# Kernel tuning notes

Measured on AMD Instinct MI355X. Metric: run time of the kernel, lower is better.

## Reference

```python
import jax, jax.numpy as jnp
import numpy as np

NEG_SLOPE = 0.2  # negative_slope of LeakyReLU

def _leaky_relu(x):
    return jnp.where(x >= 0, x, NEG_SLOPE * x)

def setup_inputs() -> dict:
    key = jax.random.key(0)
    ks = jax.random.split(key, 8)
    n_s, n_t, n_edges = 100000, 25000, 1600000
    d_s_in = d_t_in = 256
    d_s_out = d_t_out = 256
    x_source = jax.random.normal(ks[0], (n_s, d_s_in), jnp.float32)
    x_target = jax.random.normal(ks[1], (n_t, d_t_in), jnp.float32)
    # sparse neighborhood N: [n_target, n_source], COO (row=target i, col=source j)
    edge_row = jax.random.randint(ks[2], (n_edges,), 0, n_t)
    edge_col = jax.random.randint(ks[3], (n_edges,), 0, n_s)
    n_vals = jax.random.uniform(ks[4], (n_edges,), jnp.float32)
    # learnable parameters (xavier-uniform-ish scale)
    w_s = jax.random.normal(ks[5], (d_s_in, d_t_out), jnp.float32) * 0.074  # [source_in, target_out]
    w_t = jax.random.normal(ks[6], (d_t_in, d_s_out), jnp.float32) * 0.074  # [target_in, source_out]
    att_weight = jax.random.normal(ks[7], (d_t_out + d_s_out,), jnp.float32) * 0.074
    return {"x_source": x_source, "x_target": x_target, "n_vals": n_vals,
            "w_s": w_s, "w_t": w_t, "att_weight": att_weight,
            "edge_row": edge_row, "edge_col": edge_col}

def reference(x_source, x_target, n_vals, w_s, w_t, att_weight, edge_row, edge_col):
    n_s = x_source.shape[0]
    n_t = x_target.shape[0]
    d_t_out = w_s.shape[1]  # target_out_channels (split point of att_weight)
    s_msg = x_source @ w_s  # [n_s, target_out]
    t_msg = x_target @ w_t  # [n_t, source_out]
    # e_ij = LeakyReLU([s_msg_j || t_msg_i] @ a); factor the linear part per node
    a1 = att_weight[:d_t_out]   # acts on s_msg part
    a2 = att_weight[d_t_out:]   # acts on t_msg part
    p_s = s_msg @ a1            # [n_s]
    p_t = t_msg @ a2            # [n_t]
    # f on the transposed edge (i'=source=col, j'=target=row) with permuted weight
    # [a2 || a1] gives p_t[row] + p_s[col]: identical per-edge scores as e.
    ev = _leaky_relu(p_s[edge_col] + p_t[edge_row])  # [E]
    # sparse_row_norm (softmax=False): divide by row sums
    rowsum_t = jax.ops.segment_sum(ev, edge_row, num_segments=n_t)  # rows of N
    rowsum_s = jax.ops.segment_sum(ev, edge_col, num_segments=n_s)  # rows of N^T
    att_s = ev / rowsum_t[edge_row]  # A_s, aligned with N
    att_t = ev / rowsum_s[edge_col]  # A_t, aligned with N^T
    # Hadamard with N values, then sparse-dense matmul (scatter-add)
    w_e = n_vals * att_s
    w_f = n_vals * att_t
    message_on_target = jax.ops.segment_sum(w_e[:, None] * s_msg[edge_col], edge_row, num_segments=n_t)  # Y_t
    message_on_source = jax.ops.segment_sum(w_f[:, None] * t_msg[edge_row], edge_col, num_segments=n_s)  # Y_s
    # update_func=None -> identity
    return message_on_source, message_on_target
```

## Files before the change

kernel.cpp:

```cpp
#include <hip/hip_runtime.h>

#define D 256

typedef float f32x4 __attribute__((ext_vector_type(4)));

#define PROWS 32
#define PSTRIDE (D + 4)

__global__ __launch_bounds__(256) void fused_p_all(
        const float* __restrict__ xs, const float* __restrict__ ws,
        float* __restrict__ ps, unsigned short* __restrict__ xbs, int n_s, int nblk_s,
        const float* __restrict__ xt, const float* __restrict__ wt,
        float* __restrict__ pt, unsigned short* __restrict__ xbt, int n_t,
        const float* __restrict__ att) {
    __shared__ float sbuf[PROWS][PSTRIDE];
    const float* X; const float* W; float* p; unsigned short* xb;
    int M, att_off, row0;
    if (blockIdx.x < nblk_s) {
        X = xs; W = ws; p = ps; xb = xbs; M = n_s; att_off = 0;
        row0 = blockIdx.x * PROWS;
    } else {
        X = xt; W = wt; p = pt; xb = xbt; M = n_t; att_off = D;
        row0 = (blockIdx.x - nblk_s) * PROWS;
    }
    const int tid = threadIdx.x;
    for (int idx = tid; idx < PROWS * (D / 4); idx += 256) {
        int r = idx >> 6;
        int c4 = (idx & 63) * 4;
        int grow = row0 + r;
        int srcrow = grow < M ? grow : M - 1;
        *reinterpret_cast<float4*>(&sbuf[r][c4]) =
            *reinterpret_cast<const float4*>(X + (size_t)srcrow * D + c4);
    }
    __syncthreads();

    if (xb) {
        const int half = tid >> 7;
        const int c2 = (tid & 127) * 2;
        for (int r = half; r < PROWS; r += 2) {
            int row = row0 + r;
            if (row < M) {
                unsigned int u0 = __float_as_uint(sbuf[r][c2]);
                unsigned int u1 = __float_as_uint(sbuf[r][c2 + 1]);
                u0 = (u0 + 0x7FFFu + ((u0 >> 16) & 1u)) >> 16;
                u1 = (u1 + 0x7FFFu + ((u1 >> 16) & 1u)) >> 16;
                unsigned int packed = (u1 << 16) | (u0 & 0xFFFFu);
                *reinterpret_cast<unsigned int*>(xb + (size_t)row * D + c2) = packed;
            }
        }
    }

    const int g = tid >> 6;
    const int l = tid & 63;
    const int r0 = g * 8;
    float acc[8][4];
    #pragma unroll
    for (int r = 0; r < 8; ++r)
        #pragma unroll
        for (int q = 0; q < 4; ++q) acc[r][q] = 0.f;

    const float* wbase = W + 4 * l;
    for (int k8 = 0; k8 < D; k8 += 8) {
        float4 wv[8];
        #pragma unroll
        for (int kk = 0; kk < 8; ++kk)
            wv[kk] = *reinterpret_cast<const float4*>(wbase + (size_t)(k8 + kk) * D);
        #pragma unroll
        for (int h = 0; h < 2; ++h) {
            float4 xv[8];
            #pragma unroll
            for (int r = 0; r < 8; ++r)
                xv[r] = *reinterpret_cast<const float4*>(&sbuf[r0 + r][k8 + 4 * h]);
            #pragma unroll
            for (int kk = 0; kk < 4; ++kk) {
                float4 w4 = wv[4 * h + kk];
                #pragma unroll
                for (int r = 0; r < 8; ++r) {
                    float xsc = (kk == 0) ? xv[r].x : (kk == 1) ? xv[r].y
                              : (kk == 2) ? xv[r].z : xv[r].w;
                    acc[r][0] = __fmaf_rn(xsc, w4.x, acc[r][0]);
                    acc[r][1] = __fmaf_rn(xsc, w4.y, acc[r][1]);
                    acc[r][2] = __fmaf_rn(xsc, w4.z, acc[r][2]);
                    acc[r][3] = __fmaf_rn(xsc, w4.w, acc[r][3]);
                }
            }
        }
    }
    __syncthreads();
    #pragma unroll
    for (int r = 0; r < 8; ++r)
        *reinterpret_cast<float4*>(&sbuf[r0 + r][4 * l]) =
            make_float4(acc[r][0], acc[r][1], acc[r][2], acc[r][3]);
    __syncthreads();
    if (tid < PROWS) {
        int row = row0 + tid;
        if (row < M) {
            float s = 0.f;
            const float* ap = att + att_off;
            for (int j = 0; j < D; ++j) s = __fmaf_rn(sbuf[tid][j], ap[j], s);
            p[row] = s;
        }
    }
}

__global__ void count_kernel(const int* __restrict__ er, const int* __restrict__ ec,
                             int* __restrict__ cnt_t, int* __restrict__ cnt_s, int ne) {
    int e = blockIdx.x * blockDim.x + threadIdx.x;
    int st = gridDim.x * blockDim.x;
    for (; e < ne; e += st) {
        atomicAdd(&cnt_t[er[e]], 1);
        atomicAdd(&cnt_s[ec[e]], 1);
    }
}

__device__ void scan_body(const int* __restrict__ cnt, int* __restrict__ off, int n) {
    const int VPT = 16;
    __shared__ int wsum[4];
    __shared__ int s_carry;
    const int tid = threadIdx.x;
    const int lane = tid & 63, wv = tid >> 6;
    if (tid == 0) s_carry = 0;
    __syncthreads();
    for (int base = 0; base < n; base += 256 * VPT) {
        int v[VPT];
        int idx0 = base + tid * VPT;
        int tsum = 0;
        #pragma unroll
        for (int k = 0; k < VPT; ++k) {
            int id = idx0 + k;
            v[k] = (id < n) ? cnt[id] : 0;
            tsum += v[k];
        }
        int x = tsum;
        #pragma unroll
        for (int o = 1; o < 64; o <<= 1) {
            int y = __shfl_up(x, o, 64);
            if (lane >= o) x += y;
        }
        if (lane == 63) wsum[wv] = x;
        __syncthreads();
        int woff = 0;
        for (int w = 0; w < 4; ++w) if (w < wv) woff += wsum[w];
        int excl = s_carry + woff + x - tsum;
        int run = excl;
        #pragma unroll
        for (int k = 0; k < VPT; ++k) {
            int id = idx0 + k;
            if (id < n) off[id] = run;
            run += v[k];
        }
        __syncthreads();
        if (tid == 255) s_carry = excl + tsum;
        __syncthreads();
    }
    if (tid == 0) off[n] = s_carry;
}

__global__ __launch_bounds__(256) void scan2_kernel(const int* __restrict__ cnt_t,
        int* __restrict__ off_t, int n_t, const int* __restrict__ cnt_s,
        int* __restrict__ off_s, int n_s) {
    if (blockIdx.x == 0) scan_body(cnt_t, off_t, n_t);
    else scan_body(cnt_s, off_s, n_s);
}

__global__ void fill_kernel(const int* __restrict__ er, const int* __restrict__ ec,
                            const int* __restrict__ off_t, const int* __restrict__ off_s,
                            int* __restrict__ cur_t, int* __restrict__ cur_s,
                            int* __restrict__ list_t, int* __restrict__ list_s, int ne) {
    int e = blockIdx.x * blockDim.x + threadIdx.x;
    int st = gridDim.x * blockDim.x;
    for (; e < ne; e += st) {
        int r = er[e];
        int p1 = atomicAdd(&cur_t[r], 1);
        list_t[off_t[r] + p1] = e;
        int c = ec[e];
        int p2 = atomicAdd(&cur_s[c], 1);
        list_s[off_s[c] + p2] = e;
    }
}

#define MAXD 160

__global__ __launch_bounds__(64) void rowsum_weight_all(
        const int* __restrict__ off_t, int* __restrict__ list_t,
        const int* __restrict__ ecol,
        const float* __restrict__ p_t, const float* __restrict__ p_s,
        float* __restrict__ wlist_t, int n_t,
        const int* __restrict__ off_s, int* __restrict__ list_s,
        const int* __restrict__ erow,
        float* __restrict__ wlist_s, int n_s,
        const float* __restrict__ nv) {
    __shared__ int raw[MAXD];
    __shared__ int so[MAXD];
    __shared__ float sev[MAXD];
    __shared__ float snv[MAXD];
    const int bid = blockIdx.x;
    const int* off; int* list; const int* other_idx;
    const float* p_own; const float* p_other; float* wlist; int row;
    if (bid < n_t) { off = off_t; list = list_t; other_idx = ecol;
                     p_own = p_t; p_other = p_s; wlist = wlist_t; row = bid; }
    else           { off = off_s; list = list_s; other_idx = erow;
                     p_own = p_s; p_other = p_t; wlist = wlist_s; row = bid - n_t; }
    const int lane = threadIdx.x;
    const int b = off[row];
    int deg = off[row + 1] - b;
    if (deg > MAXD) deg = MAXD;

    for (int i = lane; i < deg; i += 64) raw[i] = list[b + i];
    __syncthreads();
    int myv[(MAXD + 63) / 64], myr[(MAXD + 63) / 64];
    #pragma unroll
    for (int c = 0; c < (MAXD + 63) / 64; ++c) {
        int i = lane + c * 64;
        if (i < deg) {
            int v = raw[i];
            int rank = 0;
            for (int j = 0; j < deg; ++j) rank += (raw[j] < v);
            myv[c] = v; myr[c] = rank;
        }
    }
    __syncthreads();
    #pragma unroll
    for (int c = 0; c < (MAXD + 63) / 64; ++c) {
        int i = lane + c * 64;
        if (i < deg) raw[myr[c]] = myv[c];
    }
    __syncthreads();
    const float po = p_own[row];
    for (int i = lane; i < deg; i += 64) {
        int e = raw[i];
        int o = other_idx[e];
        so[i] = o;
        float t = __fadd_rn(p_other[o], po);
        sev[i] = (t >= 0.f) ? t : __fmul_rn(0.2f, t);
        snv[i] = nv[e];
    }
    __syncthreads();
    float rs = 0.f;
    for (int i = 0; i < deg; ++i) rs = __fadd_rn(rs, sev[i]);
    for (int i = lane; i < deg; i += 64) {
        list[b + i]  = so[i];
        wlist[b + i] = __fmul_rn(snv[i], __fdiv_rn(sev[i], rs));
    }
}

__global__ __launch_bounds__(256) void gather_all_bf16(
        const int* __restrict__ off_t, const int* __restrict__ olist_t,
        const float* __restrict__ wlist_t, const unsigned short* __restrict__ xb_s,
        float* __restrict__ out_tgt, int n_t,
        const int* __restrict__ off_s, const int* __restrict__ olist_s,
        const float* __restrict__ wlist_s, const unsigned short* __restrict__ xb_t,
        float* __restrict__ out_src, int n_s) {
    const int gid = blockIdx.x * 4 + (threadIdx.x >> 6);
    if (gid >= n_t + n_s) return;
    const int lane = threadIdx.x & 63;
    const int* off; const int* ol; const float* wl;
    const unsigned short* xo; float* out; int row;
    if (gid < n_t) { off = off_t; ol = olist_t; wl = wlist_t;
                     xo = xb_s; out = out_tgt; row = gid; }
    else           { off = off_s; ol = olist_s; wl = wlist_s;
                     xo = xb_t; out = out_src; row = gid - n_t; }
    const int b = off[row];
    const int end = off[row + 1];
    const size_t eoff = (size_t)lane * 4;

    float ax = 0.f, ay = 0.f, az = 0.f, aw = 0.f;
    int i = b;
    for (; i + 8 <= end; i += 8) {
        int o[8]; float w[8]; uint2 xv[8];
        #pragma unroll
        for (int u = 0; u < 8; ++u) { o[u] = ol[i + u]; w[u] = wl[i + u]; }
        #pragma unroll
        for (int u = 0; u < 8; ++u)
            xv[u] = *reinterpret_cast<const uint2*>(xo + (size_t)o[u] * D + eoff);
        #pragma unroll
        for (int u = 0; u < 8; ++u) {
            float x0 = __uint_as_float(xv[u].x << 16);
            float x1 = __uint_as_float(xv[u].x & 0xFFFF0000u);
            float x2 = __uint_as_float(xv[u].y << 16);
            float x3 = __uint_as_float(xv[u].y & 0xFFFF0000u);
            ax = fmaf(w[u], x0, ax); ay = fmaf(w[u], x1, ay);
            az = fmaf(w[u], x2, az); aw = fmaf(w[u], x3, aw);
        }
    }
    for (; i < end; ++i) {
        int o = ol[i];
        float w = wl[i];
        uint2 xv = *reinterpret_cast<const uint2*>(xo + (size_t)o * D + eoff);
        float x0 = __uint_as_float(xv.x << 16);
        float x1 = __uint_as_float(xv.x & 0xFFFF0000u);
        float x2 = __uint_as_float(xv.y << 16);
        float x3 = __uint_as_float(xv.y & 0xFFFF0000u);
        ax = fmaf(w, x0, ax); ay = fmaf(w, x1, ay);
        az = fmaf(w, x2, az); aw = fmaf(w, x3, aw);
    }
    f32x4 r = {ax, ay, az, aw};
    __builtin_nontemporal_store(r,
        reinterpret_cast<f32x4*>(out + (size_t)row * D + eoff));
}

#define BAND 32
#define KT 8

__global__ __launch_bounds__(256) void band_gemm_all(
        float* __restrict__ Cs, const float* __restrict__ Bs_w, int nblk_s, int Ms,
        float* __restrict__ Ct, const float* __restrict__ Bt_w, int Mt) {
    __shared__ float Xs[BAND][D];
    __shared__ float Bs[KT][D];
    float* C; const float* B; int M, base_row;
    if (blockIdx.x < nblk_s) { C = Cs; B = Bs_w; M = Ms; base_row = blockIdx.x * BAND; }
    else { C = Ct; B = Bt_w; M = Mt; base_row = (blockIdx.x - nblk_s) * BAND; }
    const int tid = threadIdx.x;
    const int r0 = (tid >> 5) * 4;
    const int cA = (tid & 31) * 4;

    for (int s = tid; s < BAND * (D / 4); s += 256) {
        int row = s >> 6;
        int c4 = (s & 63) * 4;
        int grow = base_row + row;
        int srow = grow < M ? grow : M - 1;
        f32x4 v = __builtin_nontemporal_load(
            reinterpret_cast<const f32x4*>(C + (size_t)srow * D + c4));
        *reinterpret_cast<f32x4*>(&Xs[row][c4]) = v;
    }

    float acc[4][8];
    #pragma unroll
    for (int i = 0; i < 4; ++i)
        #pragma unroll
        for (int j = 0; j < 8; ++j) acc[i][j] = 0.f;

    for (int kt = 0; kt < D; kt += KT) {
        __syncthreads();
        for (int s = tid; s < KT * (D / 4); s += 256) {
            int row = s >> 6;
            int c4 = (s & 63) * 4;
            *reinterpret_cast<float4*>(&Bs[row][c4]) =
                *reinterpret_cast<const float4*>(B + (size_t)(kt + row) * D + c4);
        }
        __syncthreads();
        #pragma unroll
        for (int k4 = 0; k4 < KT; k4 += 4) {
            float4 av[4];
            #pragma unroll
            for (int i = 0; i < 4; ++i)
                av[i] = *reinterpret_cast<const float4*>(&Xs[r0 + i][kt + k4]);
            #pragma unroll
            for (int kk = 0; kk < 4; ++kk) {
                float4 blo = *reinterpret_cast<const float4*>(&Bs[k4 + kk][cA]);
                float4 bhi = *reinterpret_cast<const float4*>(&Bs[k4 + kk][cA + 128]);
                #pragma unroll
                for (int i = 0; i < 4; ++i) {
                    float a = (kk == 0) ? av[i].x : (kk == 1) ? av[i].y
                            : (kk == 2) ? av[i].z : av[i].w;
                    acc[i][0] = fmaf(a, blo.x, acc[i][0]);
                    acc[i][1] = fmaf(a, blo.y, acc[i][1]);
                    acc[i][2] = fmaf(a, blo.z, acc[i][2]);
                    acc[i][3] = fmaf(a, blo.w, acc[i][3]);
                    acc[i][4] = fmaf(a, bhi.x, acc[i][4]);
                    acc[i][5] = fmaf(a, bhi.y, acc[i][5]);
                    acc[i][6] = fmaf(a, bhi.z, acc[i][6]);
                    acc[i][7] = fmaf(a, bhi.w, acc[i][7]);
                }
            }
        }
    }
    #pragma unroll
    for (int i = 0; i < 4; ++i) {
        int row = base_row + r0 + i;
        if (row < M) {
            float* cp = C + (size_t)row * D;
            f32x4 lo = {acc[i][0], acc[i][1], acc[i][2], acc[i][3]};
            f32x4 hi = {acc[i][4], acc[i][5], acc[i][6], acc[i][7]};
            __builtin_nontemporal_store(lo, reinterpret_cast<f32x4*>(cp + cA));
            __builtin_nontemporal_store(hi, reinterpret_cast<f32x4*>(cp + cA + 128));
        }
    }
}

extern "C" void kernel_launch(void* const* d_in, const int* in_sizes, int n_in,
                              void* d_out, int out_size, void* d_ws, size_t ws_size,
                              hipStream_t stream) {
    const float* x_s = (const float*)d_in[0];
    const float* x_t = (const float*)d_in[1];
    const float* nv  = (const float*)d_in[2];
    const float* w_s = (const float*)d_in[3];
    const float* w_t = (const float*)d_in[4];
    const float* att = (const float*)d_in[5];
    const int* erow  = (const int*)d_in[6];
    const int* ecol  = (const int*)d_in[7];

    const int n_s = in_sizes[0] / D;
    const int n_t = in_sizes[1] / D;
    const int ne  = in_sizes[6];

    float* p_s      = (float*)d_ws;
    float* p_t      = p_s + n_s;
    float* wlist_t  = p_t + n_t;
    float* wlist_s  = wlist_t + ne;
    int* cnt_t  = (int*)(wlist_s + ne);
    int* cnt_s  = cnt_t + n_t;
    int* off_t  = cnt_s + n_s;
    int* off_s  = off_t + (n_t + 1);
    int* list_t = off_s + (n_s + 1);
    int* list_s = list_t + ne;
    unsigned short* xb_s = (unsigned short*)(list_s + ne);
    unsigned short* xb_t = xb_s + (size_t)n_s * D;
    size_t need = (size_t)((char*)(xb_t + (size_t)n_t * D) - (char*)d_ws);
    const bool use_bf16 = ws_size >= need;

    float* out_src = (float*)d_out;
    float* out_tgt = out_src + (size_t)n_s * D;

    (void)hipMemsetAsync(cnt_t, 0, (size_t)(n_t + n_s) * sizeof(int), stream);

    const int pblk_s = (n_s + PROWS - 1) / PROWS;
    const int pblk_t = (n_t + PROWS - 1) / PROWS;
    fused_p_all<<<pblk_s + pblk_t, 256, 0, stream>>>(
        x_s, w_s, p_s, use_bf16 ? xb_s : nullptr, n_s, pblk_s,
        x_t, w_t, p_t, use_bf16 ? xb_t : nullptr, n_t, att);

    count_kernel<<<2048, 256, 0, stream>>>(erow, ecol, cnt_t, cnt_s, ne);
    scan2_kernel<<<2, 256, 0, stream>>>(cnt_t, off_t, n_t, cnt_s, off_s, n_s);
    (void)hipMemsetAsync(cnt_t, 0, (size_t)(n_t + n_s) * sizeof(int), stream);
    fill_kernel<<<2048, 256, 0, stream>>>(erow, ecol, off_t, off_s, cnt_t, cnt_s,
                                          list_t, list_s, ne);

    rowsum_weight_all<<<n_t + n_s, 64, 0, stream>>>(off_t, list_t, ecol, p_t, p_s,
                                                    wlist_t, n_t,
                                                    off_s, list_s, erow,
                                                    wlist_s, n_s, nv);

    if (use_bf16) {
        int rows = n_t + n_s;
        gather_all_bf16<<<(rows + 3) / 4, 256, 0, stream>>>(
            off_t, list_t, wlist_t, xb_s, out_tgt, n_t,
            off_s, list_s, wlist_s, xb_t, out_src, n_s);
    }

    const int gblk_s = (n_s + BAND - 1) / BAND;
    const int gblk_t = (n_t + BAND - 1) / BAND;
    band_gemm_all<<<gblk_s + gblk_t, 256, 0, stream>>>(out_src, w_t, gblk_s, n_s,
                                                       out_tgt, w_s, n_t);
}
```

Baseline: 1.186 ms.

## Fuse edge counting into projection kernel and drop second memset

Merges the edge degree-count atomics into the projection/p-score kernel: extra leading blocks do the counting, so it overlaps with the dense projection work and one launch disappears. The projection tile shrinks to 16 rows per block with a launch-bounds occupancy hint, and fill now uses separate cursor arrays zeroed by a single larger memset, which removes the second memset between kernels. Streaming reads of edge lists and weights switch to nontemporal loads. The smaller tile reloads W more often per row, and the count blocks compete with projection blocks for CUs.

Result: slower. 1.300 ms (+9.6%).

```diff
diff --git a/kernel.cpp b/kernel.cpp
--- a/kernel.cpp
+++ b/kernel.cpp
@@ -4,24 +4,36 @@
 
 typedef float f32x4 __attribute__((ext_vector_type(4)));
 
-#define PROWS 32
+#define PROWS 16
 #define PSTRIDE (D + 4)
 
-__global__ __launch_bounds__(256) void fused_p_all(
+__global__ __launch_bounds__(256, 6) void fused_p_count(
         const float* __restrict__ xs, const float* __restrict__ ws,
         float* __restrict__ ps, unsigned short* __restrict__ xbs, int n_s, int nblk_s,
         const float* __restrict__ xt, const float* __restrict__ wt,
         float* __restrict__ pt, unsigned short* __restrict__ xbt, int n_t,
-        const float* __restrict__ att) {
+        const float* __restrict__ att,
+        const int* __restrict__ er, const int* __restrict__ ec,
+        int* __restrict__ cnt_t, int* __restrict__ cnt_s, int ne, int cb) {
     __shared__ float sbuf[PROWS][PSTRIDE];
+    if (blockIdx.x < (unsigned)cb) {
+        int e = blockIdx.x * 256 + threadIdx.x;
+        int st = cb * 256;
+        for (; e < ne; e += st) {
+            atomicAdd(&cnt_t[er[e]], 1);
+            atomicAdd(&cnt_s[ec[e]], 1);
+        }
+        return;
+    }
+    const int pbid = blockIdx.x - cb;
     const float* X; const float* W; float* p; unsigned short* xb;
     int M, att_off, row0;
-    if (blockIdx.x < nblk_s) {
+    if (pbid < nblk_s) {
         X = xs; W = ws; p = ps; xb = xbs; M = n_s; att_off = 0;
-        row0 = blockIdx.x * PROWS;
+        row0 = pbid * PROWS;
     } else {
         X = xt; W = wt; p = pt; xb = xbt; M = n_t; att_off = D;
-        row0 = (blockIdx.x - nblk_s) * PROWS;
+        row0 = (pbid - nblk_s) * PROWS;
     }
     const int tid = threadIdx.x;
     for (int idx = tid; idx < PROWS * (D / 4); idx += 256) {
@@ -52,10 +64,10 @@
 
     const int g = tid >> 6;
     const int l = tid & 63;
-    const int r0 = g * 8;
-    float acc[8][4];
-    #pragma unroll
-    for (int r = 0; r < 8; ++r)
+    const int r0 = g * 4;
+    float acc[4][4];
+    #pragma unroll
+    for (int r = 0; r < 4; ++r)
         #pragma unroll
         for (int q = 0; q < 4; ++q) acc[r][q] = 0.f;
 
@@ -67,15 +79,15 @@
             wv[kk] = *reinterpret_cast<const float4*>(wbase + (size_t)(k8 + kk) * D);
         #pragma unroll
         for (int h = 0; h < 2; ++h) {
-            float4 xv[8];
+            float4 xv[4];
             #pragma unroll
-            for (int r = 0; r < 8; ++r)
+            for (int r = 0; r < 4; ++r)
                 xv[r] = *reinterpret_cast<const float4*>(&sbuf[r0 + r][k8 + 4 * h]);
             #pragma unroll
             for (int kk = 0; kk < 4; ++kk) {
                 float4 w4 = wv[4 * h + kk];
                 #pragma unroll
-                for (int r = 0; r < 8; ++r) {
+                for (int r = 0; r < 4; ++r) {
                     float xsc = (kk == 0) ? xv[r].x : (kk == 1) ? xv[r].y
                               : (kk == 2) ? xv[r].z : xv[r].w;
                     acc[r][0] = __fmaf_rn(xsc, w4.x, acc[r][0]);
@@ -88,7 +100,7 @@
     }
     __syncthreads();
     #pragma unroll
-    for (int r = 0; r < 8; ++r)
+    for (int r = 0; r < 4; ++r)
         *reinterpret_cast<float4*>(&sbuf[r0 + r][4 * l]) =
             make_float4(acc[r][0], acc[r][1], acc[r][2], acc[r][3]);
     __syncthreads();
@@ -100,16 +112,6 @@
             for (int j = 0; j < D; ++j) s = __fmaf_rn(sbuf[tid][j], ap[j], s);
             p[row] = s;
         }
-    }
-}
-
-__global__ void count_kernel(const int* __restrict__ er, const int* __restrict__ ec,
-                             int* __restrict__ cnt_t, int* __restrict__ cnt_s, int ne) {
-    int e = blockIdx.x * blockDim.x + threadIdx.x;
-    int st = gridDim.x * blockDim.x;
-    for (; e < ne; e += st) {
-        atomicAdd(&cnt_t[er[e]], 1);
-        atomicAdd(&cnt_s[ec[e]], 1);
     }
 }
 
@@ -206,7 +208,8 @@
     int deg = off[row + 1] - b;
     if (deg > MAXD) deg = MAXD;
 
-    for (int i = lane; i < deg; i += 64) raw[i] = list[b + i];
+    for (int i = lane; i < deg; i += 64)
+        raw[i] = __builtin_nontemporal_load(list + b + i);
     __syncthreads();
     int myv[(MAXD + 63) / 64], myr[(MAXD + 63) / 64];
     #pragma unroll
@@ -233,7 +236,7 @@
         so[i] = o;
         float t = __fadd_rn(p_other[o], po);
         sev[i] = (t >= 0.f) ? t : __fmul_rn(0.2f, t);
-        snv[i] = nv[e];
+        snv[i] = __builtin_nontemporal_load(nv + e);
     }
     __syncthreads();
     float rs = 0.f;
@@ -269,7 +272,10 @@
     for (; i + 8 <= end; i += 8) {
         int o[8]; float w[8]; uint2 xv[8];
         #pragma unroll
-        for (int u = 0; u < 8; ++u) { o[u] = ol[i + u]; w[u] = wl[i + u]; }
+        for (int u = 0; u < 8; ++u) {
+            o[u] = __builtin_nontemporal_load(ol + i + u);
+            w[u] = __builtin_nontemporal_load(wl + i + u);
+        }
         #pragma unroll
         for (int u = 0; u < 8; ++u)
             xv[u] = *reinterpret_cast<const uint2*>(xo + (size_t)o[u] * D + eoff);
@@ -308,7 +314,7 @@
     __shared__ float Xs[BAND][D];
     __shared__ float Bs[KT][D];
     float* C; const float* B; int M, base_row;
-    if (blockIdx.x < nblk_s) { C = Cs; B = Bs_w; M = Ms; base_row = blockIdx.x * BAND; }
+    if (blockIdx.x < (unsigned)nblk_s) { C = Cs; B = Bs_w; M = Ms; base_row = blockIdx.x * BAND; }
     else { C = Ct; B = Bt_w; M = Mt; base_row = (blockIdx.x - nblk_s) * BAND; }
     const int tid = threadIdx.x;
     const int r0 = (tid >> 5) * 4;
@@ -400,7 +406,9 @@
     float* wlist_s  = wlist_t + ne;
     int* cnt_t  = (int*)(wlist_s + ne);
     int* cnt_s  = cnt_t + n_t;
-    int* off_t  = cnt_s + n_s;
+    int* cur_t  = cnt_s + n_s;
+    int* cur_s  = cur_t + n_t;
+    int* off_t  = cur_s + n_s;
     int* off_s  = off_t + (n_t + 1);
     int* list_t = off_s + (n_s + 1);
     int* list_s = list_t + ne;
@@ -412,18 +420,18 @@
     float* out_src = (float*)d_out;
     float* out_tgt = out_src + (size_t)n_s * D;
 
-    (void)hipMemsetAsync(cnt_t, 0, (size_t)(n_t + n_s) * sizeof(int), stream);
+    (void)hipMemsetAsync(cnt_t, 0, 2 * (size_t)(n_t + n_s) * sizeof(int), stream);
 
     const int pblk_s = (n_s + PROWS - 1) / PROWS;
     const int pblk_t = (n_t + PROWS - 1) / PROWS;
-    fused_p_all<<<pblk_s + pblk_t, 256, 0, stream>>>(
+    const int CB = 1024;
+    fused_p_count<<<CB + pblk_s + pblk_t, 256, 0, stream>>>(
         x_s, w_s, p_s, use_bf16 ? xb_s : nullptr, n_s, pblk_s,
-        x_t, w_t, p_t, use_bf16 ? xb_t : nullptr, n_t, att);
-
-    count_kernel<<<2048, 256, 0, stream>>>(erow, ecol, cnt_t, cnt_s, ne);
+        x_t, w_t, p_t, use_bf16 ? xb_t : nullptr, n_t, att,
+        erow, ecol, cnt_t, cnt_s, ne, CB);
+
     scan2_kernel<<<2, 256, 0, stream>>>(cnt_t, off_t, n_t, cnt_s, off_s, n_s);
-    (void)hipMemsetAsync(cnt_t, 0, (size_t)(n_t + n_s) * sizeof(int), stream);
-    fill_kernel<<<2048, 256, 0, stream>>>(erow, ecol, off_t, off_s, cnt_t, cnt_s,
+    fill_kernel<<<2048, 256, 0, stream>>>(erow, ecol, off_t, off_s, cur_t, cur_s,
                                           list_t, list_s, ne);
 
     rowsum_weight_all<<<n_t + n_s, 64, 0, stream>>>(off_t, list_t, ecol, p_t, p_s,
```

## Parallelize offset scan across tiles and batch gather index loads via wave shuffles

Applied to the files above, without the earlier changes.

Replaces the two-block serial prefix scan with a three-phase tiled scan (tile sums, tiny serial scan of tile sums, per-tile scan) spread over many blocks. Separate cursor arrays are zeroed alongside the counts in one memset, which removes the second memset. The gather kernel now loads 64 neighbor indices and weights per wave cooperatively and broadcasts them with shuffles, unrolling by 16 to keep more row loads in flight. Nontemporal loads are added for streaming list reads. The cost is two extra kernel launches and some shuffle overhead.

Measured after the change: 1.150 ms. 1.03x faster.

```diff
diff --git a/kernel.cpp b/kernel.cpp
--- a/kernel.cpp
+++ b/kernel.cpp
@@ -16,7 +16,7 @@
     __shared__ float sbuf[PROWS][PSTRIDE];
     const float* X; const float* W; float* p; unsigned short* xb;
     int M, att_off, row0;
-    if (blockIdx.x < nblk_s) {
+    if (blockIdx.x < (unsigned)nblk_s) {
         X = xs; W = ws; p = ps; xb = xbs; M = n_s; att_off = 0;
         row0 = blockIdx.x * PROWS;
     } else {
@@ -113,25 +113,72 @@
     }
 }
 
-__device__ void scan_body(const int* __restrict__ cnt, int* __restrict__ off, int n) {
-    const int VPT = 16;
+#define STILE 4096
+
+__global__ __launch_bounds__(256) void scanA_kernel(
+        const int* __restrict__ cnt_t, int n_t,
+        const int* __restrict__ cnt_s, int n_s,
+        int* __restrict__ tsum, int tilesT) {
+    __shared__ int wsum[4];
+    const int tid = threadIdx.x;
+    const int* src; int n, base;
+    if ((int)blockIdx.x < tilesT) { src = cnt_t; n = n_t; base = blockIdx.x * STILE; }
+    else { src = cnt_s; n = n_s; base = (blockIdx.x - tilesT) * STILE; }
+    int s = 0;
+    for (int it = 0; it < STILE; it += 1024) {
+        int idx = base + it + tid * 4;
+        if (idx + 3 < n) {
+            int4 v = *reinterpret_cast<const int4*>(src + idx);
+            s += v.x + v.y + v.z + v.w;
+        } else {
+            #pragma unroll
+            for (int k = 0; k < 4; ++k) if (idx + k < n) s += src[idx + k];
+        }
+    }
+    #pragma unroll
+    for (int o = 32; o > 0; o >>= 1) s += __shfl_xor(s, o, 64);
+    if ((tid & 63) == 0) wsum[tid >> 6] = s;
+    __syncthreads();
+    if (tid == 0) tsum[blockIdx.x] = wsum[0] + wsum[1] + wsum[2] + wsum[3];
+}
+
+__global__ void scanB_kernel(int* __restrict__ tsum, int tilesT, int tilesS,
+                             int* __restrict__ off_t, int n_t,
+                             int* __restrict__ off_s, int n_s, int ne) {
+    if (threadIdx.x == 0) {
+        int run = 0;
+        for (int i = 0; i < tilesT; ++i) { int v = tsum[i]; tsum[i] = run; run += v; }
+        run = 0;
+        for (int i = 0; i < tilesS; ++i) { int v = tsum[tilesT + i]; tsum[tilesT + i] = run; run += v; }
+        off_t[n_t] = ne;
+        off_s[n_s] = ne;
+    }
+}
+
+__global__ __launch_bounds__(256) void scanC_kernel(
+        const int* __restrict__ cnt_t, int n_t, int* __restrict__ off_t,
+        const int* __restrict__ cnt_s, int n_s, int* __restrict__ off_s,
+        const int* __restrict__ tsum, int tilesT) {
     __shared__ int wsum[4];
     __shared__ int s_carry;
     const int tid = threadIdx.x;
     const int lane = tid & 63, wv = tid >> 6;
-    if (tid == 0) s_carry = 0;
-    __syncthreads();
-    for (int base = 0; base < n; base += 256 * VPT) {
-        int v[VPT];
-        int idx0 = base + tid * VPT;
-        int tsum = 0;
-        #pragma unroll
-        for (int k = 0; k < VPT; ++k) {
-            int id = idx0 + k;
-            v[k] = (id < n) ? cnt[id] : 0;
-            tsum += v[k];
-        }
-        int x = tsum;
+    const int* src; int* dst; int n, base;
+    if ((int)blockIdx.x < tilesT) { src = cnt_t; dst = off_t; n = n_t; base = blockIdx.x * STILE; }
+    else { src = cnt_s; dst = off_s; n = n_s; base = (blockIdx.x - tilesT) * STILE; }
+    if (tid == 0) s_carry = tsum[blockIdx.x];
+    __syncthreads();
+    for (int it = 0; it < STILE; it += 1024) {
+        int idx = base + it + tid * 4;
+        int4 v = make_int4(0, 0, 0, 0);
+        if (idx + 3 < n) v = *reinterpret_cast<const int4*>(src + idx);
+        else {
+            if (idx < n)     v.x = src[idx];
+            if (idx + 1 < n) v.y = src[idx + 1];
+            if (idx + 2 < n) v.z = src[idx + 2];
+        }
+        int t4 = v.x + v.y + v.z + v.w;
+        int x = t4;
         #pragma unroll
         for (int o = 1; o < 64; o <<= 1) {
             int y = __shfl_up(x, o, 64);
@@ -141,26 +188,22 @@
         __syncthreads();
         int woff = 0;
         for (int w = 0; w < 4; ++w) if (w < wv) woff += wsum[w];
-        int excl = s_carry + woff + x - tsum;
-        int run = excl;
-        #pragma unroll
-        for (int k = 0; k < VPT; ++k) {
-            int id = idx0 + k;
-            if (id < n) off[id] = run;
-            run += v[k];
+        int excl = s_carry + woff + x - t4;
+        int4 outv;
+        outv.x = excl;
+        outv.y = excl + v.x;
+        outv.z = excl + v.x + v.y;
+        outv.w = excl + v.x + v.y + v.z;
+        if (idx + 3 < n) *reinterpret_cast<int4*>(dst + idx) = outv;
+        else {
+            if (idx < n)     dst[idx] = outv.x;
+            if (idx + 1 < n) dst[idx + 1] = outv.y;
+            if (idx + 2 < n) dst[idx + 2] = outv.z;
         }
         __syncthreads();
-        if (tid == 255) s_carry = excl + tsum;
+        if (tid == 255) s_carry = excl + t4;
         __syncthreads();
     }
-    if (tid == 0) off[n] = s_carry;
-}
-
-__global__ __launch_bounds__(256) void scan2_kernel(const int* __restrict__ cnt_t,
-        int* __restrict__ off_t, int n_t, const int* __restrict__ cnt_s,
-        int* __restrict__ off_s, int n_s) {
-    if (blockIdx.x == 0) scan_body(cnt_t, off_t, n_t);
-    else scan_body(cnt_s, off_s, n_s);
 }
 
 __global__ void fill_kernel(const int* __restrict__ er, const int* __restrict__ ec,
@@ -206,7 +249,8 @@
     int deg = off[row + 1] - b;
     if (deg > MAXD) deg = MAXD;
 
-    for (int i = lane; i < deg; i += 64) raw[i] = list[b + i];
+    for (int i = lane; i < deg; i += 64)
+        raw[i] = __builtin_nontemporal_load(list + b + i);
     __syncthreads();
     int myv[(MAXD + 63) / 64], myr[(MAXD + 63) / 64];
     #pragma unroll
@@ -233,7 +277,7 @@
         so[i] = o;
         float t = __fadd_rn(p_other[o], po);
         sev[i] = (t >= 0.f) ? t : __fmul_rn(0.2f, t);
-        snv[i] = nv[e];
+        snv[i] = __builtin_nontemporal_load(nv + e);
     }
     __syncthreads();
     float rs = 0.f;
@@ -265,34 +309,43 @@
     const size_t eoff = (size_t)lane * 4;
 
     float ax = 0.f, ay = 0.f, az = 0.f, aw = 0.f;
-    int i = b;
-    for (; i + 8 <= end; i += 8) {
-        int o[8]; float w[8]; uint2 xv[8];
-        #pragma unroll
-        for (int u = 0; u < 8; ++u) { o[u] = ol[i + u]; w[u] = wl[i + u]; }
-        #pragma unroll
-        for (int u = 0; u < 8; ++u)
-            xv[u] = *reinterpret_cast<const uint2*>(xo + (size_t)o[u] * D + eoff);
-        #pragma unroll
-        for (int u = 0; u < 8; ++u) {
-            float x0 = __uint_as_float(xv[u].x << 16);
-            float x1 = __uint_as_float(xv[u].x & 0xFFFF0000u);
-            float x2 = __uint_as_float(xv[u].y << 16);
-            float x3 = __uint_as_float(xv[u].y & 0xFFFF0000u);
-            ax = fmaf(w[u], x0, ax); ay = fmaf(w[u], x1, ay);
-            az = fmaf(w[u], x2, az); aw = fmaf(w[u], x3, aw);
-        }
-    }
-    for (; i < end; ++i) {
-        int o = ol[i];
-        float w = wl[i];
-        uint2 xv = *reinterpret_cast<const uint2*>(xo + (size_t)o * D + eoff);
-        float x0 = __uint_as_float(xv.x << 16);
-        float x1 = __uint_as_float(xv.x & 0xFFFF0000u);
-        float x2 = __uint_as_float(xv.y << 16);
-        float x3 = __uint_as_float(xv.y & 0xFFFF0000u);
-        ax = fmaf(w, x0, ax); ay = fmaf(w, x1, ay);
-        az = fmaf(w, x2, az); aw = fmaf(w, x3, aw);
+    for (int cs = b; cs < end; cs += 64) {
+        const int cn = min(64, end - cs);
+        int o_l = 0; float w_l = 0.f;
+        if (lane < cn) {
+            o_l = __builtin_nontemporal_load(ol + cs + lane);
+            w_l = __builtin_nontemporal_load(wl + cs + lane);
+        }
+        int e = 0;
+        for (; e + 16 <= cn; e += 16) {
+            float w[16]; uint2 xv[16];
+            #pragma unroll
+            for (int u = 0; u < 16; ++u) {
+                int o = __shfl(o_l, e + u, 64);
+                w[u] = __shfl(w_l, e + u, 64);
+                xv[u] = *reinterpret_cast<const uint2*>(xo + (size_t)o * D + eoff);
+            }
+            #pragma unroll
+            for (int u = 0; u < 16; ++u) {
+                float x0 = __uint_as_float(xv[u].x << 16);
+                float x1 = __uint_as_float(xv[u].x & 0xFFFF0000u);
+                float x2 = __uint_as_float(xv[u].y << 16);
+                float x3 = __uint_as_float(xv[u].y & 0xFFFF0000u);
+                ax = fmaf(w[u], x0, ax); ay = fmaf(w[u], x1, ay);
+                az = fmaf(w[u], x2, az); aw = fmaf(w[u], x3, aw);
+            }
+        }
+        for (; e < cn; ++e) {
+            int o = __shfl(o_l, e, 64);
+            float w = __shfl(w_l, e, 64);
+            uint2 xv = *reinterpret_cast<const uint2*>(xo + (size_t)o * D + eoff);
+            float x0 = __uint_as_float(xv.x << 16);
+            float x1 = __uint_as_float(xv.x & 0xFFFF0000u);
+            float x2 = __uint_as_float(xv.y << 16);
+            float x3 = __uint_as_float(xv.y & 0xFFFF0000u);
+            ax = fmaf(w, x0, ax); ay = fmaf(w, x1, ay);
+            az = fmaf(w, x2, az); aw = fmaf(w, x3, aw);
+        }
     }
     f32x4 r = {ax, ay, az, aw};
     __builtin_nontemporal_store(r,
@@ -308,7 +361,7 @@
     __shared__ float Xs[BAND][D];
     __shared__ float Bs[KT][D];
     float* C; const float* B; int M, base_row;
-    if (blockIdx.x < nblk_s) { C = Cs; B = Bs_w; M = Ms; base_row = blockIdx.x * BAND; }
+    if (blockIdx.x < (unsigned)nblk_s) { C = Cs; B = Bs_w; M = Ms; base_row = blockIdx.x * BAND; }
     else { C = Ct; B = Bt_w; M = Mt; base_row = (blockIdx.x - nblk_s) * BAND; }
     const int tid = threadIdx.x;
     const int r0 = (tid >> 5) * 4;
@@ -400,9 +453,12 @@
     float* wlist_s  = wlist_t + ne;
     int* cnt_t  = (int*)(wlist_s + ne);
     int* cnt_s  = cnt_t + n_t;
-    int* off_t  = cnt_s + n_s;
+    int* cur_t  = cnt_s + n_s;
+    int* cur_s  = cur_t + n_t;
+    int* off_t  = cur_s + n_s;
     int* off_s  = off_t + (n_t + 1);
-    int* list_t = off_s + (n_s + 1);
+    int* tsum   = off_s + (n_s + 1);
+    int* list_t = tsum + 64;
     int* list_s = list_t + ne;
     unsigned short* xb_s = (unsigned short*)(list_s + ne);
     unsigned short* xb_t = xb_s + (size_t)n_s * D;
@@ -412,7 +468,7 @@
     float* out_src = (float*)d_out;
     float* out_tgt = out_src + (size_t)n_s * D;
 
-    (void)hipMemsetAsync(cnt_t, 0, (size_t)(n_t + n_s) * sizeof(int), stream);
+    (void)hipMemsetAsync(cnt_t, 0, 2 * (size_t)(n_t + n_s) * sizeof(int), stream);
 
     const int pblk_s = (n_s + PROWS - 1) / PROWS;
     const int pblk_t = (n_t + PROWS - 1) / PROWS;
@@ -421,9 +477,18 @@
         x_t, w_t, p_t, use_bf16 ? xb_t : nullptr, n_t, att);
 
     count_kernel<<<2048, 256, 0, stream>>>(erow, ecol, cnt_t, cnt_s, ne);
-    scan2_kernel<<<2, 256, 0, stream>>>(cnt_t, off_t, n_t, cnt_s, off_s, n_s);
-    (void)hipMemsetAsync(cnt_t, 0, (size_t)(n_t + n_s) * sizeof(int), stream);
-    fill_kernel<<<2048, 256, 0, stream>>>(erow, ecol, off_t, off_s, cnt_t, cnt_s,
+
+    const int tilesT = (n_t + STILE - 1) / STILE;
+    const int tilesS = (n_s + STILE - 1) / STILE;
+    scanA_kernel<<<tilesT + tilesS, 256, 0, stream>>>(cnt_t, n_t, cnt_s, n_s,
+                                                      tsum, tilesT);
+    scanB_kernel<<<1, 64, 0, stream>>>(tsum, tilesT, tilesS,
+                                       off_t, n_t, off_s, n_s, ne);
+    scanC_kernel<<<tilesT + tilesS, 256, 0, stream>>>(cnt_t, n_t, off_t,
+                                                      cnt_s, n_s, off_s,
+                                                      tsum, tilesT);
+
+    fill_kernel<<<2048, 256, 0, stream>>>(erow, ecol, off_t, off_s, cur_t, cur_s,
                                           list_t, list_s, ne);
 
     rowsum_weight_all<<<n_t + n_s, 64, 0, stream>>>(off_t, list_t, ecol, p_t, p_s,
```
